# Kernel optimization log

Hardware: AMD Instinct MI355X
Metric: run time of the kernel (lower is better)

The kernel has to match this reference:

```python
import jax, jax.numpy as jnp
import numpy as np


def setup_inputs() -> dict:
    key = jax.random.key(0)
    kx, ky = jax.random.split(key)
    B, C, D, H, W = 2, 16, 64, 128, 128
    x = jax.random.normal(kx, (B, C, D, H, W), dtype=jnp.float32)
    y = jax.random.randint(ky, (B, D, H, W), 0, C, dtype=jnp.int64)
    return {"x": x, "y": y}


def reference(x, y):
    # x: [B,C,D,H,W] logits, y: [B,D,H,W] int labels in [0,C)
    B, C = x.shape[0], x.shape[1]
    logp = jax.nn.log_softmax(x, axis=1)                      # [B,C,D,H,W]
    # per-voxel NLL = CrossEntropyLoss(reduction='none')
    nll = -jnp.take_along_axis(logp, y[:, None], axis=1)[:, 0]  # [B,D,H,W]

    # fuse the B*C masked means into one segment reduction over (b, class)
    nll_flat = nll.reshape(-1)                                # [B*N]
    seg = (jnp.arange(B, dtype=y.dtype)[:, None] * C + y.reshape(B, -1)).reshape(-1)
    sums = jax.ops.segment_sum(nll_flat, seg, num_segments=B * C)
    counts = jax.ops.segment_sum(jnp.ones_like(nll_flat), seg, num_segments=B * C)
    # classes absent in a sample contribute 0 (matches `if m.any()`)
    means = jnp.where(counts > 0, sums / jnp.maximum(counts, 1.0), 0.0)  # [B*C]
    r = means.reshape(B, C).sum(axis=1) / C                   # [B]
    return r.mean()
```

## Files before the change

### kernel.cpp

```cpp
#include <hip/hip_runtime.h>

#define BB 2
#define CC 16
#define NVOX (64 * 128 * 128)
#define N4   (NVOX / 4)

__global__ void cwce_init(float* __restrict__ ws_sum, unsigned* __restrict__ ws_cnt) {
    int t = threadIdx.x;
    if (t < BB * CC) { ws_sum[t] = 0.0f; ws_cnt[t] = 0u; }
}

__global__ __launch_bounds__(256) void cwce_main(const float* __restrict__ x,
                                                 const int* __restrict__ y,
                                                 float* __restrict__ ws_sum,
                                                 unsigned* __restrict__ ws_cnt) {
    __shared__ float    s_sum[CC];
    __shared__ unsigned s_cnt[CC];
    const int t = threadIdx.x;
    if (t < CC) { s_sum[t] = 0.0f; s_cnt[t] = 0u; }
    __syncthreads();

    const unsigned gid = blockIdx.x * 256u + t;
    const unsigned b   = gid >> 18;
    const unsigned n4  = gid & (N4 - 1);

    const float4* xb = (const float4*)x + (size_t)(b * CC) * N4 + n4;
    const int4 lab4 = ((const int4*)y)[gid];

    float xv[CC][4];
#pragma unroll
    for (int c = 0; c < CC; ++c) {
        float4 v = xb[(size_t)c * N4];
        xv[c][0] = v.x; xv[c][1] = v.y; xv[c][2] = v.z; xv[c][3] = v.w;
    }
    const int labs[4] = {lab4.x, lab4.y, lab4.z, lab4.w};

#pragma unroll
    for (int j = 0; j < 4; ++j) {
        float m = xv[0][j];
#pragma unroll
        for (int c = 1; c < CC; ++c) m = fmaxf(m, xv[c][j]);
        const int lj = labs[j];
        float s = 0.0f, xy = 0.0f;
#pragma unroll
        for (int c = 0; c < CC; ++c) {
            s += __expf(xv[c][j] - m);
            if (c == lj) xy = xv[c][j];
        }
        const float nll = m + __logf(s) - xy;
        atomicAdd(&s_sum[lj], nll);
        atomicAdd(&s_cnt[lj], 1u);
    }
    __syncthreads();

    if (t < CC) {
        atomicAdd(&ws_sum[b * CC + t], s_sum[t]);
        atomicAdd(&ws_cnt[b * CC + t], s_cnt[t]);
    }
}

__global__ void cwce_final(const float* __restrict__ ws_sum,
                           const unsigned* __restrict__ ws_cnt,
                           float* __restrict__ out) {
    const int t = threadIdx.x;
    float v = 0.0f;
    if (t < BB * CC) {
        const unsigned c = ws_cnt[t];
        v = (c > 0u) ? (ws_sum[t] / (float)c) : 0.0f;
    }
#pragma unroll
    for (int off = 32; off >= 1; off >>= 1) v += __shfl_down(v, off);
    if (t == 0) out[0] = v * (1.0f / (BB * CC));
}

extern "C" void kernel_launch(void* const* d_in, const int* in_sizes, int n_in,
                              void* d_out, int out_size, void* d_ws, size_t ws_size,
                              hipStream_t stream) {
    const float* x = (const float*)d_in[0];
    const int*   y = (const int*)d_in[1];
    float*       out = (float*)d_out;

    float*    ws_sum = (float*)d_ws;
    unsigned* ws_cnt = (unsigned*)(ws_sum + BB * CC);

    cwce_init<<<1, 64, 0, stream>>>(ws_sum, ws_cnt);
    cwce_main<<<2048, 256, 0, stream>>>(x, y, ws_sum, ws_cnt);
    cwce_final<<<1, 64, 0, stream>>>(ws_sum, ws_cnt, out);
}
```

Before: 200.7 us.

## Replace global atomics with per-block partials and use nontemporal loads

```diff
diff --git a/kernel.cpp b/kernel.cpp
--- a/kernel.cpp
+++ b/kernel.cpp
@@ -2,18 +2,17 @@
 
 #define BB 2
 #define CC 16
+#define SEGS (BB * CC)
 #define NVOX (64 * 128 * 128)
 #define N4   (NVOX / 4)
+#define NBLK 2048
 
-__global__ void cwce_init(float* __restrict__ ws_sum, unsigned* __restrict__ ws_cnt) {
-    int t = threadIdx.x;
-    if (t < BB * CC) { ws_sum[t] = 0.0f; ws_cnt[t] = 0u; }
-}
+typedef float v4f __attribute__((ext_vector_type(4)));
 
 __global__ __launch_bounds__(256) void cwce_main(const float* __restrict__ x,
                                                  const int* __restrict__ y,
-                                                 float* __restrict__ ws_sum,
-                                                 unsigned* __restrict__ ws_cnt) {
+                                                 float* __restrict__ part_sum,
+                                                 unsigned* __restrict__ part_cnt) {
     __shared__ float    s_sum[CC];
     __shared__ unsigned s_cnt[CC];
     const int t = threadIdx.x;
@@ -24,13 +23,13 @@
     const unsigned b   = gid >> 18;
     const unsigned n4  = gid & (N4 - 1);
 
-    const float4* xb = (const float4*)x + (size_t)(b * CC) * N4 + n4;
+    const v4f* xb = (const v4f*)x + (size_t)(b * CC) * N4 + n4;
     const int4 lab4 = ((const int4*)y)[gid];
 
     float xv[CC][4];
 #pragma unroll
     for (int c = 0; c < CC; ++c) {
-        float4 v = xb[(size_t)c * N4];
+        v4f v = __builtin_nontemporal_load(xb + (size_t)c * N4);
         xv[c][0] = v.x; xv[c][1] = v.y; xv[c][2] = v.z; xv[c][3] = v.w;
     }
     const int labs[4] = {lab4.x, lab4.y, lab4.z, lab4.w};
@@ -54,23 +53,41 @@
     __syncthreads();
 
     if (t < CC) {
-        atomicAdd(&ws_sum[b * CC + t], s_sum[t]);
-        atomicAdd(&ws_cnt[b * CC + t], s_cnt[t]);
+        part_sum[blockIdx.x * CC + t] = s_sum[t];
+        part_cnt[blockIdx.x * CC + t] = s_cnt[t];
     }
 }
 
-__global__ void cwce_final(const float* __restrict__ ws_sum,
-                           const unsigned* __restrict__ ws_cnt,
+__global__ void cwce_final(const float* __restrict__ part_sum,
+                           const unsigned* __restrict__ part_cnt,
                            float* __restrict__ out) {
+    __shared__ float fs[16][CC];
+    __shared__ float fc[16][CC];
     const int t = threadIdx.x;
-    float v = 0.0f;
-    if (t < BB * CC) {
-        const unsigned c = ws_cnt[t];
-        v = (c > 0u) ? (ws_sum[t] / (float)c) : 0.0f;
+    const int c = t & 15;
+    const int g = t >> 4;
+    float s = 0.0f, n = 0.0f;
+    for (int r = g * 128; r < (g + 1) * 128; ++r) {
+        s += part_sum[r * CC + c];
+        n += (float)part_cnt[r * CC + c];
     }
+    fs[g][c] = s;
+    fc[g][c] = n;
+    __syncthreads();
+
+    if (t < 64) {
+        float v = 0.0f;
+        if (t < SEGS) {
+            const int b = t >> 4;
+            float ts = 0.0f, tn = 0.0f;
 #pragma unroll
-    for (int off = 32; off >= 1; off >>= 1) v += __shfl_down(v, off);
-    if (t == 0) out[0] = v * (1.0f / (BB * CC));
+            for (int k = 0; k < 8; ++k) { ts += fs[b * 8 + k][c]; tn += fc[b * 8 + k][c]; }
+            v = (tn > 0.0f) ? (ts / tn) : 0.0f;
+        }
+#pragma unroll
+        for (int off = 32; off >= 1; off >>= 1) v += __shfl_down(v, off);
+        if (t == 0) out[0] = v * (1.0f / SEGS);
+    }
 }
 
 extern "C" void kernel_launch(void* const* d_in, const int* in_sizes, int n_in,
@@ -80,10 +97,9 @@
     const int*   y = (const int*)d_in[1];
     float*       out = (float*)d_out;
 
-    float*    ws_sum = (float*)d_ws;
-    unsigned* ws_cnt = (unsigned*)(ws_sum + BB * CC);
+    float*    part_sum = (float*)d_ws;
+    unsigned* part_cnt = (unsigned*)(part_sum + NBLK * CC);
 
-    cwce_init<<<1, 64, 0, stream>>>(ws_sum, ws_cnt);
-    cwce_main<<<2048, 256, 0, stream>>>(x, y, ws_sum, ws_cnt);
-    cwce_final<<<1, 64, 0, stream>>>(ws_sum, ws_cnt, out);
+    cwce_main<<<NBLK, 256, 0, stream>>>(x, y, part_sum, part_cnt);
+    cwce_final<<<1, 256, 0, stream>>>(part_sum, part_cnt, out);
 }
```

New measurement: 196.8 us. No clear change (-1.9%).
